# Kernel tuning notes

Hardware: AMD Instinct MI355X
Metric: run time of the kernel (lower is better)

The kernel has to match this reference:

```python
import jax, jax.numpy as jnp
import numpy as np

N = 100000   # nodes
E = 1600000  # edges (avg degree 16)
D = 64       # hidden_dim == in_channels
EPS = 1e-15  # PyG DGI epsilon


def gcn_conv(x, W, b, row, col, n):
    h = x @ W                                                    # [n, D]
    deg = jax.ops.segment_sum(jnp.ones(row.shape[0], x.dtype), col,
                              num_segments=n) + 1.0              # +1 for self-loop
    dis = jax.lax.rsqrt(deg)                                     # deg^-1/2
    norm = dis[row] * dis[col]                                   # [E]
    agg = jax.ops.segment_sum(h[row] * norm[:, None], col, num_segments=n)
    return agg + h * (dis * dis)[:, None] + b                    # self-loop term + bias


def encode(x, row, col, W1, b1, W2, b2, n):
    h = jax.nn.relu(gcn_conv(x, W1, b1, row, col, n))
    return gcn_conv(h, W2, b2, row, col, n)


def setup_inputs() -> dict:
    key = jax.random.key(0)
    k = jax.random.split(key, 8)
    s = 1.0 / np.sqrt(D)
    return {
        "x": jax.random.normal(k[0], (N, D), jnp.float32),
        "W1": jax.random.uniform(k[1], (D, D), jnp.float32, -s, s),
        "b1": jnp.zeros((D,), jnp.float32),
        "W2": jax.random.uniform(k[2], (D, D), jnp.float32, -s, s),
        "b2": jnp.zeros((D,), jnp.float32),
        "W_dgi": jax.random.uniform(k[3], (D, D), jnp.float32, -s, s),
        "edge_index": jax.random.randint(k[4], (2, E), 0, N, jnp.int32),
        "perm": jax.random.permutation(k[5], N).astype(jnp.int32),
    }


def reference(x, W1, b1, W2, b2, W_dgi, edge_index, perm):
    row, col = edge_index[0], edge_index[1]
    pos_z = encode(x, row, col, W1, b1, W2, b2, N)          # [N, D]
    neg_z = encode(x[perm], row, col, W1, b1, W2, b2, N)    # corrupted features, same graph
    summary = jax.nn.sigmoid(pos_z.mean(axis=0))            # [D]
    ws = W_dgi @ summary                                    # [D]
    pos_p = jax.nn.sigmoid(pos_z @ ws)                      # [N]
    neg_p = jax.nn.sigmoid(neg_z @ ws)                      # [N]
    pos_loss = -jnp.log(pos_p + EPS).mean()
    neg_loss = -jnp.log(1.0 - neg_p + EPS).mean()
    return pos_loss + neg_loss
```

## Files before the change

kernel.cpp:

```cpp
#include <hip/hip_runtime.h>
#include <hip/hip_bf16.h>
#include <math.h>

#define GG 2048
#define RB 32
#define NB_SHIFT 9
#define NPB 512
#define BINCAP 10240
#define BINREGION 12288
#define PCHUNK 2048

typedef __hip_bfloat16 bf16;
typedef unsigned int uint;
typedef unsigned short ushort;
typedef unsigned char uchar;
typedef short bf16x8 __attribute__((ext_vector_type(8)));
typedef float f32x4 __attribute__((ext_vector_type(4)));
typedef float f32x2 __attribute__((ext_vector_type(2)));

__device__ __forceinline__ bf16  f2b(float x) { return __float2bfloat16(x); }
__device__ __forceinline__ short f2bs(float x) {
    bf16 b = __float2bfloat16(x);
    return *reinterpret_cast<short*>(&b);
}
__device__ __forceinline__ ushort packfp8(float p, float n) {
    return (ushort)__builtin_amdgcn_cvt_pk_fp8_f32(p, n, 0, false);
}
__device__ __forceinline__ f32x2 unpackfp8(uint u) {
    return __builtin_amdgcn_cvt_pk_f32_fp8((int)u, false);
}
__device__ __forceinline__ f32x2 unpackfp8_hi(uint u) {
    return __builtin_amdgcn_cvt_pk_f32_fp8((int)u, true);
}

__global__ void zero_kernel(int* __restrict__ bincnt, float* __restrict__ lossacc,
                            int* __restrict__ flags, int nb) {
    int i = threadIdx.x;
    if (i < nb) bincnt[i] = 0;
    if (i < 2) { lossacc[i] = 0.f; flags[i] = 0; }
}

__global__ __launch_bounds__(256) void partition_edges(
        const int* __restrict__ row, const int* __restrict__ col,
        uint* __restrict__ bins, int* __restrict__ bincnt, int E, int nb) {
    __shared__ int lcnt[256];
    __shared__ int lbase[256];
    for (int chunk = blockIdx.x * PCHUNK; chunk < E; chunk += gridDim.x * PCHUNK) {
        int end = chunk + PCHUNK < E ? chunk + PCHUNK : E;
        if (threadIdx.x < nb) lcnt[threadIdx.x] = 0;
        __syncthreads();
        for (int e = chunk + threadIdx.x; e < end; e += 256)
            atomicAdd(&lcnt[col[e] >> NB_SHIFT], 1);
        __syncthreads();
        if (threadIdx.x < nb) {
            lbase[threadIdx.x] = atomicAdd(&bincnt[threadIdx.x], lcnt[threadIdx.x]);
            lcnt[threadIdx.x] = 0;
        }
        __syncthreads();
        for (int e = chunk + threadIdx.x; e < end; e += 256) {
            int c = col[e], r = row[e];
            int g = c >> NB_SHIFT;
            int dst = lbase[g] + atomicAdd(&lcnt[g], 1);
            if (dst < BINCAP)
                bins[(size_t)g * BINCAP + dst] = ((uint)r << NB_SHIFT) | (uint)(c & (NPB - 1));
        }
        __syncthreads();
    }
}

__global__ __launch_bounds__(256) void place_lds(
        const uint* __restrict__ bins, const int* __restrict__ bincnt,
        int* __restrict__ bucket, int* __restrict__ off, int* __restrict__ cnt,
        int N) {
    __shared__ int lcnt[NPB];
    __shared__ int s[NPB];
    __shared__ int win[BINREGION];
    int b  = blockIdx.x;
    int lo = b << NB_SHIFT;
    int base = b * BINREGION;
    int ne = bincnt[b];
    if (ne > BINCAP) ne = BINCAP;
    const uint* be = bins + (size_t)b * BINCAP;
    for (int i = threadIdx.x; i < NPB; i += 256) lcnt[i] = 0;
    __syncthreads();
    for (int i = threadIdx.x; i < ne; i += 256)
        atomicAdd(&lcnt[be[i] & (NPB - 1)], 1);
    __syncthreads();
    int i0 = threadIdx.x, i1 = threadIdx.x + 256;
    s[i0] = (lcnt[i0] + 3) & ~3;
    s[i1] = (lcnt[i1] + 3) & ~3;
    __syncthreads();
    for (int st = 1; st < NPB; st <<= 1) {
        int v0 = i0 >= st ? s[i0 - st] : 0;
        int v1 = i1 >= st ? s[i1 - st] : 0;
        __syncthreads();
        s[i0] += v0; s[i1] += v1;
        __syncthreads();
    }
    for (int i = threadIdx.x; i < NPB; i += 256) {
        int v = lo + i;
        int pc = (lcnt[i] + 3) & ~3;
        int start = s[i] - pc;
        if (v < N) { off[v] = base + start; cnt[v] = lcnt[i]; }
        lcnt[i] = start;
    }
    __syncthreads();
    for (int i = threadIdx.x; i < ne; i += 256) {
        uint u = be[i];
        int slot = atomicAdd(&lcnt[u & (NPB - 1)], 1);
        if (slot < BINREGION) win[slot] = (int)(u >> NB_SHIFT);
    }
    __syncthreads();
    int wsize = s[NPB - 1];
    if (wsize > BINREGION) wsize = BINREGION;
    for (int i = threadIdx.x * 4; i < wsize; i += 1024)
        *(int4*)&bucket[base + i] = *(const int4*)&win[i];
}

__global__ __launch_bounds__(256) void gemm1_mfma(
        const float* __restrict__ X, const float* __restrict__ W,
        const int* __restrict__ perm, const int* __restrict__ cnt,
        ushort* __restrict__ out, int n) {
    int lane = threadIdx.x & 63, wid = threadIdx.x >> 6;
    int l15 = lane & 15, lg = lane >> 4;
    bf16x8 bfr[2][4];
#pragma unroll
    for (int kt = 0; kt < 2; kt++)
#pragma unroll
        for (int nt = 0; nt < 4; nt++)
#pragma unroll
            for (int i = 0; i < 8; i++)
                bfr[kt][nt][i] = f2bs(W[(kt * 32 + lg * 8 + i) * 64 + nt * 16 + l15]);
    int ntiles = (n + 15) >> 4;
    for (int t = blockIdx.x * 4 + wid; t < ntiles; t += gridDim.x * 4) {
        int rowA = t * 16 + l15;
        if (rowA >= n) rowA = n - 1;
        int prow = perm[rowA];
        const float4* xp = (const float4*)(X + (size_t)rowA * 64);
        const float4* xn = (const float4*)(X + (size_t)prow * 64);
        bf16x8 ap[2], an[2];
#pragma unroll
        for (int kt = 0; kt < 2; kt++) {
            float4 p0 = xp[kt * 8 + lg * 2], p1 = xp[kt * 8 + lg * 2 + 1];
            float4 n0 = xn[kt * 8 + lg * 2], n1 = xn[kt * 8 + lg * 2 + 1];
            ap[kt][0] = f2bs(p0.x); ap[kt][1] = f2bs(p0.y);
            ap[kt][2] = f2bs(p0.z); ap[kt][3] = f2bs(p0.w);
            ap[kt][4] = f2bs(p1.x); ap[kt][5] = f2bs(p1.y);
            ap[kt][6] = f2bs(p1.z); ap[kt][7] = f2bs(p1.w);
            an[kt][0] = f2bs(n0.x); an[kt][1] = f2bs(n0.y);
            an[kt][2] = f2bs(n0.z); an[kt][3] = f2bs(n0.w);
            an[kt][4] = f2bs(n1.x); an[kt][5] = f2bs(n1.y);
            an[kt][6] = f2bs(n1.z); an[kt][7] = f2bs(n1.w);
        }
        f32x4 accp[4], accn[4];
#pragma unroll
        for (int nt = 0; nt < 4; nt++) { accp[nt] = (f32x4)0.f; accn[nt] = (f32x4)0.f; }
#pragma unroll
        for (int nt = 0; nt < 4; nt++) {
            accp[nt] = __builtin_amdgcn_mfma_f32_16x16x32_bf16(ap[0], bfr[0][nt], accp[nt], 0, 0, 0);
            accp[nt] = __builtin_amdgcn_mfma_f32_16x16x32_bf16(ap[1], bfr[1][nt], accp[nt], 0, 0, 0);
            accn[nt] = __builtin_amdgcn_mfma_f32_16x16x32_bf16(an[0], bfr[0][nt], accn[nt], 0, 0, 0);
            accn[nt] = __builtin_amdgcn_mfma_f32_16x16x32_bf16(an[1], bfr[1][nt], accn[nt], 0, 0, 0);
        }
        float dvr[4];
#pragma unroll
        for (int reg = 0; reg < 4; reg++) {
            int node = t * 16 + lg * 4 + reg;
            dvr[reg] = node < n ? rsqrtf((float)cnt[node] + 1.0f) : 0.f;
        }
#pragma unroll
        for (int nt = 0; nt < 4; nt++)
#pragma unroll
            for (int reg = 0; reg < 4; reg++) {
                int node = t * 16 + lg * 4 + reg;
                if (node < n)
                    out[(size_t)node * 64 + nt * 16 + l15] =
                        packfp8(accp[nt][reg] * dvr[reg], accn[nt][reg] * dvr[reg]);
            }
    }
}

__global__ __launch_bounds__(256) void gemm2_mfma(
        const ushort* __restrict__ H, const float* __restrict__ W,
        const int* __restrict__ cnt, ushort* __restrict__ out, int n) {
    int lane = threadIdx.x & 63, wid = threadIdx.x >> 6;
    int l15 = lane & 15, lg = lane >> 4;
    bf16x8 bfr[2][4];
#pragma unroll
    for (int kt = 0; kt < 2; kt++)
#pragma unroll
        for (int nt = 0; nt < 4; nt++)
#pragma unroll
            for (int i = 0; i < 8; i++)
                bfr[kt][nt][i] = f2bs(W[(kt * 32 + lg * 8 + i) * 64 + nt * 16 + l15]);
    int ntiles = (n + 15) >> 4;
    for (int t = blockIdx.x * 4 + wid; t < ntiles; t += gridDim.x * 4) {
        int rowA = t * 16 + l15;
        if (rowA >= n) rowA = n - 1;
        const uint4* h = (const uint4*)(H + (size_t)rowA * 64);
        bf16x8 ap[2], an[2];
#pragma unroll
        for (int kt = 0; kt < 2; kt++) {
            uint4 hh = h[kt * 4 + lg];
            uint uu[4] = {hh.x, hh.y, hh.z, hh.w};
#pragma unroll
            for (int j = 0; j < 4; j++) {
                f32x2 lo = unpackfp8(uu[j]);
                f32x2 hi = unpackfp8_hi(uu[j]);
                ap[kt][2 * j]     = f2bs(lo.x); an[kt][2 * j]     = f2bs(lo.y);
                ap[kt][2 * j + 1] = f2bs(hi.x); an[kt][2 * j + 1] = f2bs(hi.y);
            }
        }
        f32x4 accp[4], accn[4];
#pragma unroll
        for (int nt = 0; nt < 4; nt++) { accp[nt] = (f32x4)0.f; accn[nt] = (f32x4)0.f; }
#pragma unroll
        for (int nt = 0; nt < 4; nt++) {
            accp[nt] = __builtin_amdgcn_mfma_f32_16x16x32_bf16(ap[0], bfr[0][nt], accp[nt], 0, 0, 0);
            accp[nt] = __builtin_amdgcn_mfma_f32_16x16x32_bf16(ap[1], bfr[1][nt], accp[nt], 0, 0, 0);
            accn[nt] = __builtin_amdgcn_mfma_f32_16x16x32_bf16(an[0], bfr[0][nt], accn[nt], 0, 0, 0);
            accn[nt] = __builtin_amdgcn_mfma_f32_16x16x32_bf16(an[1], bfr[1][nt], accn[nt], 0, 0, 0);
        }
        float dvr[4];
#pragma unroll
        for (int reg = 0; reg < 4; reg++) {
            int node = t * 16 + lg * 4 + reg;
            dvr[reg] = node < n ? rsqrtf((float)cnt[node] + 1.0f) : 0.f;
        }
#pragma unroll
        for (int nt = 0; nt < 4; nt++)
#pragma unroll
            for (int reg = 0; reg < 4; reg++) {
                int node = t * 16 + lg * 4 + reg;
                if (node < n)
                    out[(size_t)node * 64 + nt * 16 + l15] =
                        packfp8(accp[nt][reg] * dvr[reg], accn[nt][reg] * dvr[reg]);
            }
    }
}

template <int MODE>
__global__ __launch_bounds__(256) void conv_packed(
        const ushort* __restrict__ g, const int* __restrict__ bucket,
        const int* __restrict__ off, const int* __restrict__ cnt,
        const float* __restrict__ bias,
        ushort* __restrict__ out, float* __restrict__ colpart, int n) {
    int lane = threadIdx.x & 63, wid = threadIdx.x >> 6;
    const uchar* gb = (const uchar*)g;
    uint l2 = (uint)lane * 2;
    __shared__ float s[256];
    float colp  = 0.f;
    float blane = bias[lane];
    int wstart = blockIdx.x * 4 + wid, wstride = gridDim.x * 4;
    for (int v = wstart; v < n; v += wstride) {
        int vu  = __builtin_amdgcn_readfirstlane(v);
        int c   = cnt[vu];
        int ofs = off[vu];
        float dv = rsqrtf((float)c + 1.0f);
        f32x2 acc0 = unpackfp8(*(const ushort*)(gb + ((size_t)(uint)vu << 7) + l2));
        f32x2 acc1 = {0.f, 0.f}, acc2 = {0.f, 0.f}, acc3 = {0.f, 0.f};
        f32x2 acc4 = {0.f, 0.f}, acc5 = {0.f, 0.f}, acc6 = {0.f, 0.f}, acc7 = {0.f, 0.f};
        const int*  bk  = bucket + ofs;
        const int4* bk4 = (const int4*)bk;
        int nq16 = c >> 4;
        for (int q = 0; q < nq16; q++) {
            int4 ra = bk4[4 * q],     rb = bk4[4 * q + 1];
            int4 rc = bk4[4 * q + 2], rd = bk4[4 * q + 3];
            uint u0  = *(const ushort*)(gb + ((size_t)(uint)ra.x << 7) + l2);
            uint u1  = *(const ushort*)(gb + ((size_t)(uint)ra.y << 7) + l2);
            uint u2  = *(const ushort*)(gb + ((size_t)(uint)ra.z << 7) + l2);
            uint u3  = *(const ushort*)(gb + ((size_t)(uint)ra.w << 7) + l2);
            uint u4  = *(const ushort*)(gb + ((size_t)(uint)rb.x << 7) + l2);
            uint u5  = *(const ushort*)(gb + ((size_t)(uint)rb.y << 7) + l2);
            uint u6  = *(const ushort*)(gb + ((size_t)(uint)rb.z << 7) + l2);
            uint u7  = *(const ushort*)(gb + ((size_t)(uint)rb.w << 7) + l2);
            uint u8  = *(const ushort*)(gb + ((size_t)(uint)rc.x << 7) + l2);
            uint u9  = *(const ushort*)(gb + ((size_t)(uint)rc.y << 7) + l2);
            uint u10 = *(const ushort*)(gb + ((size_t)(uint)rc.z << 7) + l2);
            uint u11 = *(const ushort*)(gb + ((size_t)(uint)rc.w << 7) + l2);
            uint u12 = *(const ushort*)(gb + ((size_t)(uint)rd.x << 7) + l2);
            uint u13 = *(const ushort*)(gb + ((size_t)(uint)rd.y << 7) + l2);
            uint u14 = *(const ushort*)(gb + ((size_t)(uint)rd.z << 7) + l2);
            uint u15 = *(const ushort*)(gb + ((size_t)(uint)rd.w << 7) + l2);
            acc0 += unpackfp8(u0);  acc1 += unpackfp8(u1);
            acc2 += unpackfp8(u2);  acc3 += unpackfp8(u3);
            acc4 += unpackfp8(u4);  acc5 += unpackfp8(u5);
            acc6 += unpackfp8(u6);  acc7 += unpackfp8(u7);
            acc0 += unpackfp8(u8);  acc1 += unpackfp8(u9);
            acc2 += unpackfp8(u10); acc3 += unpackfp8(u11);
            acc4 += unpackfp8(u12); acc5 += unpackfp8(u13);
            acc6 += unpackfp8(u14); acc7 += unpackfp8(u15);
        }
        int i = nq16 << 4;
        for (; i + 4 <= c; i += 4) {
            int4 r = *(const int4*)(bk + i);
            acc0 += unpackfp8(*(const ushort*)(gb + ((size_t)(uint)r.x << 7) + l2));
            acc1 += unpackfp8(*(const ushort*)(gb + ((size_t)(uint)r.y << 7) + l2));
            acc2 += unpackfp8(*(const ushort*)(gb + ((size_t)(uint)r.z << 7) + l2));
            acc3 += unpackfp8(*(const ushort*)(gb + ((size_t)(uint)r.w << 7) + l2));
        }
        for (; i < c; i++) {
            int r = bk[i];
            acc0 += unpackfp8(*(const ushort*)(gb + ((size_t)(uint)r << 7) + l2));
        }
        f32x2 acc = ((acc0 + acc1) + (acc2 + acc3)) + ((acc4 + acc5) + (acc6 + acc7));
        float rp = fmaf(dv, acc.x, blane);
        float rn = fmaf(dv, acc.y, blane);
        size_t vo = (size_t)vu * 64 + lane;
        if (MODE == 0) {
            out[vo] = packfp8(fmaxf(rp, 0.f), fmaxf(rn, 0.f));
        } else {
            out[vo] = packfp8(rp, rn);
            colp += rp;
        }
    }
    if (MODE == 1) {
        s[wid * 64 + lane] = colp;
        __syncthreads();
        if (wid == 0) {
            float t = s[lane] + s[64 + lane] + s[128 + lane] + s[192 + lane];
            colpart[(size_t)blockIdx.x * 64 + lane] = t;
        }
    }
}

__global__ __launch_bounds__(256) void colreduce_summary(
        const float* __restrict__ colpart, float* __restrict__ colpart2,
        const float* __restrict__ Wdgi, float* __restrict__ wsv,
        int* __restrict__ flag, float invN) {
    int lane = threadIdx.x & 63, w = threadIdx.x >> 6;
    __shared__ float s4[4][64];
    __shared__ int tk;
    float t = 0.f;
    int base = blockIdx.x * RB;
    for (int g = w; g < RB; g += 4) t += colpart[(size_t)(base + g) * 64 + lane];
    s4[w][lane] = t;
    __syncthreads();
    if (w == 0)
        colpart2[(size_t)blockIdx.x * 64 + lane] =
            s4[0][lane] + s4[1][lane] + s4[2][lane] + s4[3][lane];
    __threadfence();
    if (threadIdx.x == 0) tk = atomicAdd(flag, 1);
    __syncthreads();
    if (tk == (int)gridDim.x - 1) {
        __threadfence();
        __shared__ float sm[64];
        __shared__ float p4[4][64];
        float u = 0.f;
        for (int g = w; g < (int)gridDim.x; g += 4)
            u += colpart2[(size_t)g * 64 + lane];
        p4[w][lane] = u;
        __syncthreads();
        if (w == 0) {
            u = p4[0][lane] + p4[1][lane] + p4[2][lane] + p4[3][lane];
            sm[lane] = 1.f / (1.f + expf(-u * invN));
        }
        __syncthreads();
        if (threadIdx.x < 64) {
            float a = 0.f;
            for (int j = 0; j < 64; j++) a += Wdgi[threadIdx.x * 64 + j] * sm[j];
            wsv[threadIdx.x] = a;
        }
    }
}

__global__ __launch_bounds__(256) void loss4_kernel(
        const ushort* __restrict__ z, const float* __restrict__ wsv,
        float* __restrict__ lossacc, int n) {
    int lane = threadIdx.x & 63, wid = threadIdx.x >> 6;
    int sub = lane >> 4, dch = lane & 15;
    __shared__ float s[16];
    float w0 = wsv[dch * 4], w1 = wsv[dch * 4 + 1];
    float w2 = wsv[dch * 4 + 2], w3 = wsv[dch * 4 + 3];
    float lp = 0.f, ln = 0.f;
    int nq = (n + 3) >> 2;
    for (int qi = blockIdx.x * 4 + wid; qi < nq; qi += gridDim.x * 4) {
        int v = qi * 4 + sub;
        float p = 0.f, q = 0.f;
        if (v < n) {
            uint2 u = *(const uint2*)(z + (size_t)v * 64 + dch * 4);
            f32x2 a0 = unpackfp8(u.x), a1 = unpackfp8_hi(u.x);
            f32x2 a2 = unpackfp8(u.y), a3 = unpackfp8_hi(u.y);
            p = a0.x * w0 + a1.x * w1 + a2.x * w2 + a3.x * w3;
            q = a0.y * w0 + a1.y * w1 + a2.y * w2 + a3.y * w3;
        }
        for (int o = 1; o < 16; o <<= 1) {
            p += __shfl_xor(p, o, 64);
            q += __shfl_xor(q, o, 64);
        }
        if (dch == 0 && v < n) {
            lp += -logf(1.f / (1.f + expf(-p)) + 1e-15f);
            ln += -logf(1.f / (1.f + expf( q)) + 1e-15f);
        }
    }
    lp += __shfl_xor(lp, 16, 64); ln += __shfl_xor(ln, 16, 64);
    lp += __shfl_xor(lp, 32, 64); ln += __shfl_xor(ln, 32, 64);
    if (lane == 0) { s[wid] = lp; s[8 + wid] = ln; }
    __syncthreads();
    if (threadIdx.x == 0) atomicAdd(&lossacc[0], s[0] + s[1] + s[2] + s[3]);
    if (threadIdx.x == 1) atomicAdd(&lossacc[1], s[8] + s[9] + s[10] + s[11]);
}

__global__ void finalize_kernel(const float* __restrict__ lossacc,
                                float* __restrict__ out, float invN) {
    out[0] = (lossacc[0] + lossacc[1]) * invN;
}

extern "C" void kernel_launch(void* const* d_in, const int* in_sizes, int n_in,
                              void* d_out, int out_size, void* d_ws, size_t ws_size,
                              hipStream_t stream) {
    const float* x    = (const float*)d_in[0];
    const float* W1   = (const float*)d_in[1];
    const float* b1   = (const float*)d_in[2];
    const float* W2   = (const float*)d_in[3];
    const float* b2   = (const float*)d_in[4];
    const float* Wdgi = (const float*)d_in[5];
    const int*   edge = (const int*)d_in[6];
    const int*   perm = (const int*)d_in[7];

    const int N = in_sizes[7];
    const int E = in_sizes[6] / 2;
    const int* row = edge;
    const int* col = edge + E;
    const int nb = (N + NPB - 1) >> NB_SHIFT;

    char* wsb = (char*)d_ws;
    size_t woff = 0;
    auto alloc = [&](size_t bytes) -> void* {
        void* p = wsb + woff;
        woff = (woff + bytes + 255) & ~(size_t)255;
        return p;
    };
    int*    bucket   = (int*)  alloc((size_t)nb * BINREGION * 4);
    uint*   bins     = (uint*) alloc((size_t)nb * BINCAP * 4);
    int*    bincnt   = (int*)  alloc((size_t)nb * 4);
    int*    cnt      = (int*)  alloc((size_t)N * 4);
    int*    off      = (int*)  alloc((size_t)N * 4);
    ushort* G        = (ushort*)alloc((size_t)N * 64 * 2);
    ushort* H        = (ushort*)alloc((size_t)N * 64 * 2);
    float*  colpart  = (float*)alloc((size_t)GG * 64 * 4);
    float*  colpart2 = (float*)alloc((size_t)(GG / RB) * 64 * 4);
    float*  wsv      = (float*)alloc(64 * 4);
    float*  lossacc  = (float*)alloc(2 * 4);
    int*    flags    = (int*)  alloc(2 * 4);

    zero_kernel<<<1, 256, 0, stream>>>(bincnt, lossacc, flags, nb);

    const int nchunks = (E + PCHUNK - 1) / PCHUNK;
    partition_edges<<<nchunks, 256, 0, stream>>>(row, col, bins, bincnt, E, nb);
    place_lds<<<nb, 256, 0, stream>>>(bins, bincnt, bucket, off, cnt, N);

    gemm1_mfma<<<1024, 256, 0, stream>>>(x, W1, perm, cnt, G, N);
    conv_packed<0><<<GG, 256, 0, stream>>>(G, bucket, off, cnt, b1, H, nullptr, N);
    gemm2_mfma<<<1024, 256, 0, stream>>>(H, W2, cnt, G, N);
    conv_packed<1><<<GG, 256, 0, stream>>>(G, bucket, off, cnt, b2, H, colpart, N);

    colreduce_summary<<<GG / RB, 256, 0, stream>>>(colpart, colpart2, Wdgi, wsv,
                                                   &flags[0], 1.0f / N);
    loss4_kernel<<<1024, 256, 0, stream>>>(H, wsv, lossacc, N);
    finalize_kernel<<<1, 1, 0, stream>>>(lossacc, (float*)d_out, 1.0f / N);
}
```

Before: 202.8 us.

## Replace second GCN aggregation with scalar projection before neighbor sum

Exploits linearity of the second GCN layer. The column mean of pos_z is computed as a weighted column sum of the pre-aggregation features, using per-node weights w built from the degree normalization in place_lds. The final logits then come from projecting each node's features onto ws first and aggregating only scalar pairs over neighbors. This replaces the 64-wide second gather with a float2 gather, at the cost of an extra atomic-heavy weight pass, a new tdot kernel and float atomics that make the summation order nondeterministic.

New measurement: 369.5 us. 82.2% more time.

```diff
diff --git a/kernel.cpp b/kernel.cpp
--- a/kernel.cpp
+++ b/kernel.cpp
@@ -3,12 +3,12 @@
 #include <math.h>
 
 #define GG 2048
-#define RB 32
 #define NB_SHIFT 9
 #define NPB 512
 #define BINCAP 10240
 #define BINREGION 12288
 #define PCHUNK 2048
+#define CSB 64
 
 typedef __hip_bfloat16 bf16;
 typedef unsigned int uint;
@@ -33,11 +33,13 @@
     return __builtin_amdgcn_cvt_pk_f32_fp8((int)u, true);
 }
 
-__global__ void zero_kernel(int* __restrict__ bincnt, float* __restrict__ lossacc,
-                            int* __restrict__ flags, int nb) {
-    int i = threadIdx.x;
-    if (i < nb) bincnt[i] = 0;
-    if (i < 2) { lossacc[i] = 0.f; flags[i] = 0; }
+__global__ __launch_bounds__(256) void zero_kernel(
+        float* __restrict__ w, int* __restrict__ bincnt,
+        float* __restrict__ lossacc, int* __restrict__ flags, int nb, int n) {
+    int tid = blockIdx.x * 256 + threadIdx.x;
+    for (int i = tid; i < n; i += gridDim.x * 256) w[i] = 0.f;
+    if (tid < nb) bincnt[tid] = 0;
+    if (tid < 2) { lossacc[tid] = 0.f; flags[tid] = 0; }
 }
 
 __global__ __launch_bounds__(256) void partition_edges(
@@ -71,7 +73,7 @@
 __global__ __launch_bounds__(256) void place_lds(
         const uint* __restrict__ bins, const int* __restrict__ bincnt,
         int* __restrict__ bucket, int* __restrict__ off, int* __restrict__ cnt,
-        int N) {
+        float* __restrict__ w, int N) {
     __shared__ int lcnt[NPB];
     __shared__ int s[NPB];
     __shared__ int win[BINREGION];
@@ -86,6 +88,11 @@
     for (int i = threadIdx.x; i < ne; i += 256)
         atomicAdd(&lcnt[be[i] & (NPB - 1)], 1);
     __syncthreads();
+    for (int i = threadIdx.x; i < ne; i += 256) {
+        uint u = be[i];
+        atomicAdd(&w[(int)(u >> NB_SHIFT)],
+                  rsqrtf((float)lcnt[u & (NPB - 1)] + 1.0f));
+    }
     int i0 = threadIdx.x, i1 = threadIdx.x + 256;
     s[i0] = (lcnt[i0] + 3) & ~3;
     s[i1] = (lcnt[i1] + 3) & ~3;
@@ -239,17 +246,13 @@
     }
 }
 
-template <int MODE>
 __global__ __launch_bounds__(256) void conv_packed(
         const ushort* __restrict__ g, const int* __restrict__ bucket,
         const int* __restrict__ off, const int* __restrict__ cnt,
-        const float* __restrict__ bias,
-        ushort* __restrict__ out, float* __restrict__ colpart, int n) {
+        const float* __restrict__ bias, ushort* __restrict__ out, int n) {
     int lane = threadIdx.x & 63, wid = threadIdx.x >> 6;
     const uchar* gb = (const uchar*)g;
     uint l2 = (uint)lane * 2;
-    __shared__ float s[256];
-    float colp  = 0.f;
     float blane = bias[lane];
     int wstart = blockIdx.x * 4 + wid, wstride = gridDim.x * 4;
     for (int v = wstart; v < n; v += wstride) {
@@ -306,38 +309,28 @@
         f32x2 acc = ((acc0 + acc1) + (acc2 + acc3)) + ((acc4 + acc5) + (acc6 + acc7));
         float rp = fmaf(dv, acc.x, blane);
         float rn = fmaf(dv, acc.y, blane);
-        size_t vo = (size_t)vu * 64 + lane;
-        if (MODE == 0) {
-            out[vo] = packfp8(fmaxf(rp, 0.f), fmaxf(rn, 0.f));
-        } else {
-            out[vo] = packfp8(rp, rn);
-            colp += rp;
-        }
-    }
-    if (MODE == 1) {
-        s[wid * 64 + lane] = colp;
-        __syncthreads();
-        if (wid == 0) {
-            float t = s[lane] + s[64 + lane] + s[128 + lane] + s[192 + lane];
-            colpart[(size_t)blockIdx.x * 64 + lane] = t;
-        }
-    }
-}
-
-__global__ __launch_bounds__(256) void colreduce_summary(
-        const float* __restrict__ colpart, float* __restrict__ colpart2,
-        const float* __restrict__ Wdgi, float* __restrict__ wsv,
-        int* __restrict__ flag, float invN) {
-    int lane = threadIdx.x & 63, w = threadIdx.x >> 6;
+        out[(size_t)vu * 64 + lane] = packfp8(fmaxf(rp, 0.f), fmaxf(rn, 0.f));
+    }
+}
+
+__global__ __launch_bounds__(256) void colsumw_kernel(
+        const ushort* __restrict__ g2, const float* __restrict__ w,
+        const int* __restrict__ cnt, const float* __restrict__ b2,
+        const float* __restrict__ Wdgi, float* __restrict__ part,
+        float* __restrict__ wsv, int* __restrict__ flag, int n, float invN) {
+    int lane = threadIdx.x & 63, wid = threadIdx.x >> 6;
     __shared__ float s4[4][64];
     __shared__ int tk;
-    float t = 0.f;
-    int base = blockIdx.x * RB;
-    for (int g = w; g < RB; g += 4) t += colpart[(size_t)(base + g) * 64 + lane];
-    s4[w][lane] = t;
-    __syncthreads();
-    if (w == 0)
-        colpart2[(size_t)blockIdx.x * 64 + lane] =
+    float acc = 0.f;
+    for (int u = blockIdx.x * 4 + wid; u < n; u += gridDim.x * 4) {
+        float wf = w[u] + rsqrtf((float)cnt[u] + 1.0f);
+        f32x2 d = unpackfp8(*(const ushort*)(g2 + (size_t)u * 64 + lane));
+        acc = fmaf(d.x, wf, acc);
+    }
+    s4[wid][lane] = acc;
+    __syncthreads();
+    if (wid == 0)
+        part[(size_t)blockIdx.x * 64 + lane] =
             s4[0][lane] + s4[1][lane] + s4[2][lane] + s4[3][lane];
     __threadfence();
     if (threadIdx.x == 0) tk = atomicAdd(flag, 1);
@@ -345,40 +338,46 @@
     if (tk == (int)gridDim.x - 1) {
         __threadfence();
         __shared__ float sm[64];
-        __shared__ float p4[4][64];
-        float u = 0.f;
-        for (int g = w; g < (int)gridDim.x; g += 4)
-            u += colpart2[(size_t)g * 64 + lane];
-        p4[w][lane] = u;
-        __syncthreads();
-        if (w == 0) {
-            u = p4[0][lane] + p4[1][lane] + p4[2][lane] + p4[3][lane];
-            sm[lane] = 1.f / (1.f + expf(-u * invN));
+        __shared__ float ws[64];
+        float u2 = 0.f;
+        for (int g = wid; g < (int)gridDim.x; g += 4)
+            u2 += part[(size_t)g * 64 + lane];
+        s4[wid][lane] = u2;
+        __syncthreads();
+        if (wid == 0) {
+            u2 = s4[0][lane] + s4[1][lane] + s4[2][lane] + s4[3][lane];
+            float mean = fmaf(u2, invN, b2[lane]);
+            sm[lane] = 1.f / (1.f + expf(-mean));
         }
         __syncthreads();
         if (threadIdx.x < 64) {
             float a = 0.f;
             for (int j = 0; j < 64; j++) a += Wdgi[threadIdx.x * 64 + j] * sm[j];
+            ws[threadIdx.x] = a;
             wsv[threadIdx.x] = a;
         }
-    }
-}
-
-__global__ __launch_bounds__(256) void loss4_kernel(
-        const ushort* __restrict__ z, const float* __restrict__ wsv,
-        float* __restrict__ lossacc, int n) {
+        __syncthreads();
+        if (threadIdx.x == 0) {
+            float b = 0.f;
+            for (int j = 0; j < 64; j++) b += b2[j] * ws[j];
+            wsv[64] = b;
+        }
+    }
+}
+
+__global__ __launch_bounds__(256) void tdot_kernel(
+        const ushort* __restrict__ g2, const float* __restrict__ wsv,
+        float2* __restrict__ t2, int n) {
     int lane = threadIdx.x & 63, wid = threadIdx.x >> 6;
     int sub = lane >> 4, dch = lane & 15;
-    __shared__ float s[16];
     float w0 = wsv[dch * 4], w1 = wsv[dch * 4 + 1];
     float w2 = wsv[dch * 4 + 2], w3 = wsv[dch * 4 + 3];
-    float lp = 0.f, ln = 0.f;
     int nq = (n + 3) >> 2;
     for (int qi = blockIdx.x * 4 + wid; qi < nq; qi += gridDim.x * 4) {
         int v = qi * 4 + sub;
         float p = 0.f, q = 0.f;
         if (v < n) {
-            uint2 u = *(const uint2*)(z + (size_t)v * 64 + dch * 4);
+            uint2 u = *(const uint2*)(g2 + (size_t)v * 64 + dch * 4);
             f32x2 a0 = unpackfp8(u.x), a1 = unpackfp8_hi(u.x);
             f32x2 a2 = unpackfp8(u.y), a3 = unpackfp8_hi(u.y);
             p = a0.x * w0 + a1.x * w1 + a2.x * w2 + a3.x * w3;
@@ -388,17 +387,53 @@
             p += __shfl_xor(p, o, 64);
             q += __shfl_xor(q, o, 64);
         }
-        if (dch == 0 && v < n) {
-            lp += -logf(1.f / (1.f + expf(-p)) + 1e-15f);
-            ln += -logf(1.f / (1.f + expf( q)) + 1e-15f);
-        }
-    }
-    lp += __shfl_xor(lp, 16, 64); ln += __shfl_xor(ln, 16, 64);
-    lp += __shfl_xor(lp, 32, 64); ln += __shfl_xor(ln, 32, 64);
-    if (lane == 0) { s[wid] = lp; s[8 + wid] = ln; }
-    __syncthreads();
-    if (threadIdx.x == 0) atomicAdd(&lossacc[0], s[0] + s[1] + s[2] + s[3]);
-    if (threadIdx.x == 1) atomicAdd(&lossacc[1], s[8] + s[9] + s[10] + s[11]);
+        if (dch == 0 && v < n) t2[v] = make_float2(p, q);
+    }
+}
+
+__global__ __launch_bounds__(256) void convloss_kernel(
+        const float2* __restrict__ t2, const int* __restrict__ bucket,
+        const int* __restrict__ off, const int* __restrict__ cnt,
+        const float* __restrict__ wsv, float* __restrict__ lossacc, int n) {
+    __shared__ float s[512];
+    float b2ws = wsv[64];
+    float lp = 0.f, ln = 0.f;
+    for (int v = blockIdx.x * 256 + threadIdx.x; v < n; v += gridDim.x * 256) {
+        int c   = cnt[v];
+        int ofs = off[v];
+        float dv = rsqrtf((float)c + 1.0f);
+        float2 st = t2[v];
+        float sp = st.x, sn = st.y;
+        const int* bk = bucket + ofs;
+        int i = 0;
+        for (; i + 4 <= c; i += 4) {
+            int4 r = *(const int4*)(bk + i);
+            float2 a0 = t2[r.x], a1 = t2[r.y], a2 = t2[r.z], a3 = t2[r.w];
+            sp += (a0.x + a1.x) + (a2.x + a3.x);
+            sn += (a0.y + a1.y) + (a2.y + a3.y);
+        }
+        for (; i < c; i++) {
+            float2 a = t2[bk[i]];
+            sp += a.x;
+            sn += a.y;
+        }
+        float p = fmaf(dv, sp, b2ws);
+        float q = fmaf(dv, sn, b2ws);
+        lp += -logf(1.f / (1.f + expf(-p)) + 1e-15f);
+        ln += -logf(1.f / (1.f + expf( q)) + 1e-15f);
+    }
+    s[threadIdx.x] = lp;
+    s[256 + threadIdx.x] = ln;
+    __syncthreads();
+    for (int st2 = 128; st2; st2 >>= 1) {
+        if (threadIdx.x < st2) {
+            s[threadIdx.x] += s[threadIdx.x + st2];
+            s[256 + threadIdx.x] += s[256 + threadIdx.x + st2];
+        }
+        __syncthreads();
+    }
+    if (threadIdx.x == 0) atomicAdd(&lossacc[0], s[0]);
+    if (threadIdx.x == 1) atomicAdd(&lossacc[1], s[256]);
 }
 
 __global__ void finalize_kernel(const float* __restrict__ lossacc,
@@ -431,32 +466,33 @@
         woff = (woff + bytes + 255) & ~(size_t)255;
         return p;
     };
-    int*    bucket   = (int*)  alloc((size_t)nb * BINREGION * 4);
-    uint*   bins     = (uint*) alloc((size_t)nb * BINCAP * 4);
-    int*    bincnt   = (int*)  alloc((size_t)nb * 4);
-    int*    cnt      = (int*)  alloc((size_t)N * 4);
-    int*    off      = (int*)  alloc((size_t)N * 4);
+    int*    bucket   = (int*)   alloc((size_t)nb * BINREGION * 4);
+    uint*   bins     = (uint*)  alloc((size_t)nb * BINCAP * 4);
+    int*    bincnt   = (int*)   alloc((size_t)nb * 4);
+    int*    cnt      = (int*)   alloc((size_t)N * 4);
+    int*    off      = (int*)   alloc((size_t)N * 4);
+    float*  w        = (float*) alloc((size_t)N * 4);
     ushort* G        = (ushort*)alloc((size_t)N * 64 * 2);
     ushort* H        = (ushort*)alloc((size_t)N * 64 * 2);
-    float*  colpart  = (float*)alloc((size_t)GG * 64 * 4);
-    float*  colpart2 = (float*)alloc((size_t)(GG / RB) * 64 * 4);
-    float*  wsv      = (float*)alloc(64 * 4);
-    float*  lossacc  = (float*)alloc(2 * 4);
-    int*    flags    = (int*)  alloc(2 * 4);
-
-    zero_kernel<<<1, 256, 0, stream>>>(bincnt, lossacc, flags, nb);
+    float2* t2       = (float2*)alloc((size_t)N * 8);
+    float*  part     = (float*) alloc((size_t)CSB * 64 * 4);
+    float*  wsv      = (float*) alloc(72 * 4);
+    float*  lossacc  = (float*) alloc(2 * 4);
+    int*    flags    = (int*)   alloc(2 * 4);
+
+    zero_kernel<<<128, 256, 0, stream>>>(w, bincnt, lossacc, flags, nb, N);
 
     const int nchunks = (E + PCHUNK - 1) / PCHUNK;
     partition_edges<<<nchunks, 256, 0, stream>>>(row, col, bins, bincnt, E, nb);
-    place_lds<<<nb, 256, 0, stream>>>(bins, bincnt, bucket, off, cnt, N);
+    place_lds<<<nb, 256, 0, stream>>>(bins, bincnt, bucket, off, cnt, w, N);
 
     gemm1_mfma<<<1024, 256, 0, stream>>>(x, W1, perm, cnt, G, N);
-    conv_packed<0><<<GG, 256, 0, stream>>>(G, bucket, off, cnt, b1, H, nullptr, N);
+    conv_packed<<<GG, 256, 0, stream>>>(G, bucket, off, cnt, b1, H, N);
     gemm2_mfma<<<1024, 256, 0, stream>>>(H, W2, cnt, G, N);
-    conv_packed<1><<<GG, 256, 0, stream>>>(G, bucket, off, cnt, b2, H, colpart, N);
-
-    colreduce_summary<<<GG / RB, 256, 0, stream>>>(colpart, colpart2, Wdgi, wsv,
-                                                   &flags[0], 1.0f / N);
-    loss4_kernel<<<1024, 256, 0, stream>>>(H, wsv, lossacc, N);
+
+    colsumw_kernel<<<CSB, 256, 0, stream>>>(G, w, cnt, b2, Wdgi, part, wsv,
+                                            &flags[0], N, 1.0f / N);
+    tdot_kernel<<<512, 256, 0, stream>>>(G, wsv, t2, N);
+    convloss_kernel<<<392, 256, 0, stream>>>(t2, bucket, off, cnt, wsv, lossacc, N);
     finalize_kernel<<<1, 1, 0, stream>>>(lossacc, (float*)d_out, 1.0f / N);
 }
```
